# Performance work log

Measured on AMD Instinct MI355X. Metric: run time of the kernel, lower is better.

Reference implementation:

```python
import jax, jax.numpy as jnp
import numpy as np

ORDER = 2
M = 3  # number_timeseries


def setup_inputs() -> dict:
    key = jax.random.key(0)
    ks = jax.random.split(key, 8)
    N, T = 256, 4096
    H, OUT = 128, 10
    d_phi_in = (ORDER + 1) * M          # 9
    d_rho_in = ORDER * M + H            # 134
    s = lambda fan_in: 1.0 / np.sqrt(fan_in)
    return {
        "x": jax.random.normal(ks[0], (N, M * T), dtype=jnp.float32),
        "phi_w1": jax.random.normal(ks[1], (d_phi_in, H), dtype=jnp.float32) * s(d_phi_in),
        "phi_b1": jnp.zeros((H,), jnp.float32),
        "phi_w2": jax.random.normal(ks[2], (H, H), dtype=jnp.float32) * s(H),
        "phi_b2": jnp.zeros((H,), jnp.float32),
        "phi_w3": jax.random.normal(ks[3], (H, H), dtype=jnp.float32) * s(H),
        "phi_b3": jnp.zeros((H,), jnp.float32),
        "rho_w1": jax.random.normal(ks[4], (d_rho_in, H), dtype=jnp.float32) * s(d_rho_in),
        "rho_b1": jnp.zeros((H,), jnp.float32),
        "rho_w2": jax.random.normal(ks[5], (H, OUT), dtype=jnp.float32) * s(H),
        "rho_b2": jnp.zeros((OUT,), jnp.float32),
    }


def reference(x, phi_w1, phi_b1, phi_w2, phi_b2, phi_w3, phi_b3,
              rho_w1, rho_b1, rho_w2, rho_b2):
    N = x.shape[0]
    xr = x.reshape(N, M, -1)                      # (N, M, T)
    T = xr.shape[-1]
    L = T - ORDER                                 # number of windows
    # cat over lags along channel dim, then transpose -> (N, L, (ORDER+1)*M)
    input_inner = jnp.concatenate(
        [xr[:, :, i:L + i] for i in range(ORDER + 1)], axis=1
    ).swapaxes(1, 2)                              # (N, L, 9)
    h = jax.nn.relu(input_inner @ phi_w1 + phi_b1)
    h = jax.nn.relu(h @ phi_w2 + phi_b2)
    h = h @ phi_w3 + phi_b3                       # (N, L, 128)
    output_inner = jnp.sum(h, axis=1)             # (N, 128)
    input_outer = jnp.concatenate(
        [xr[:, :, :ORDER].reshape(N, -1), output_inner], axis=1
    )                                             # (N, 134)
    g = jax.nn.relu(input_outer @ rho_w1 + rho_b1)
    return g @ rho_w2 + rho_b2                    # (N, 10)
```

## Files before the change

kernel.cpp:

```cpp
#include <hip/hip_runtime.h>
#include <hip/hip_bf16.h>


#define NN 256
#define MM 3
#define TT 4096
#define LL 4094
#define HH 128
#define CHUNKS 4
#define STAGES 4
#define RPS 256
#define XROW 24

#define WS_W1 (512 * 1024)
#define WS_W2 (512 * 1024 + 8192)

typedef __attribute__((ext_vector_type(8))) short bf16x8;
typedef __attribute__((ext_vector_type(4))) float f32x4;
typedef __attribute__((ext_vector_type(4))) unsigned short u16x4;
typedef __attribute__((ext_vector_type(4))) unsigned int u32x4;

__device__ __forceinline__ unsigned short f2bf(float x) {
    __hip_bfloat16 h = __float2bfloat16(x);
    union { __hip_bfloat16 h; unsigned short u; } v; v.h = h;
    return v.u;
}

__global__ void pen_prep(const float* __restrict__ w1, const float* __restrict__ b1,
                         const float* __restrict__ w2,
                         unsigned short* __restrict__ w1t,
                         unsigned short* __restrict__ w2t)
{
    const int tid = threadIdx.x;
    for (int idx = tid; idx < 512; idx += 256) {
        const int cf = idx >> 6, lane = idx & 63;
        const int lq = lane >> 4, lr = lane & 15;
        const int chan = 32 * (cf >> 1) + 8 * (lr >> 2) + 4 * (cf & 1) + (lr & 3);
        #pragma unroll
        for (int e = 0; e < 8; ++e) {
            const int k = 8 * lq + e;
            float v = 0.f;
            if (k < 9)       v = w1[k * HH + chan];
            else if (k == 9) v = b1[chan];
            w1t[idx * 8 + e] = f2bf(v);
        }
    }
    for (int idx = tid; idx < 2048; idx += 256) {
        const int lane = idx & 63;
        const int kk = (idx >> 6) & 3, of = (idx >> 8) & 3, oh = idx >> 10;
        const int lq = lane >> 4, lr = lane & 15;
        const int o = oh * 64 + of * 16 + lr;
        #pragma unroll
        for (int e = 0; e < 8; ++e) {
            const int i = 32 * kk + 8 * lq + e;
            w2t[idx * 8 + e] = f2bf(w2[i * HH + o]);
        }
    }
}

__global__ __launch_bounds__(256, 2) void pen_inner(
    const float* __restrict__ x,
    const float* __restrict__ b2,
    const unsigned short* __restrict__ w1t,
    const unsigned short* __restrict__ w2t,
    float* __restrict__ partials)
{
    __shared__ __align__(16) unsigned short xw[XROW * RPS + 32];
    __shared__ float red[2][HH];

    const int tid  = threadIdx.x;
    const int wave = tid >> 6;
    const int lane = tid & 63;
    const int lr   = lane & 15;
    const int lq   = lane >> 4;
    const int rg   = wave >> 1;
    const int oh   = wave & 1;

    const int bx    = blockIdx.x;
    const int n     = bx >> 2;
    const int chunk = bx & 3;

    const float* xn = x + n * (MM * TT);

    bf16x8 w1f[8];
    #pragma unroll
    for (int cf = 0; cf < 8; ++cf)
        w1f[cf] = *(const bf16x8*)&w1t[(cf * 64 + lane) * 8];
    bf16x8 w2f[4][4];
    #pragma unroll
    for (int of = 0; of < 4; ++of)
        #pragma unroll
        for (int kk = 0; kk < 4; ++kk)
            w2f[of][kk] = *(const bf16x8*)&w2t[(((oh * 4 + of) * 4 + kk) * 64 + lane) * 8];
    f32x4 b2f[4];
    #pragma unroll
    for (int of = 0; of < 4; ++of)
        #pragma unroll
        for (int j = 0; j < 4; ++j)
            b2f[of][j] = b2[oh * 64 + of * 16 + lq * 4 + j];

    if (tid < 32) xw[XROW * RPS + tid] = 0;

    const f32x4 zero4 = {0.f, 0.f, 0.f, 0.f};
    const int xo = XROW * lr + 8 * lq;
    float colsum[4][4] = {{0,0,0,0},{0,0,0,0},{0,0,0,0},{0,0,0,0}};

    for (int st = 0; st < STAGES; ++st) {
        __syncthreads();

        {
            const int r = tid;
            const int rowg = chunk * 1024 + st * 256 + r;
            unsigned short kv[9];
            #pragma unroll
            for (int k = 0; k < 9; ++k) {
                const int i = k / 3;
                const int m = k - i * 3;
                const int t = rowg + i;
                kv[k] = (t < TT) ? f2bf(xn[m * TT + t]) : (unsigned short)0;
            }
            u16x4 s0, s1, s2;
            s0[0] = kv[0]; s0[1] = kv[1]; s0[2] = kv[2]; s0[3] = kv[3];
            s1[0] = kv[4]; s1[1] = kv[5]; s1[2] = kv[6]; s1[3] = kv[7];
            s2[0] = kv[8]; s2[1] = 0x3F80; s2[2] = 0; s2[3] = 0;
            u16x4 z; z[0] = 0; z[1] = 0; z[2] = 0; z[3] = 0;
            *(u16x4*)&xw[XROW * r]      = s0;
            *(u16x4*)&xw[XROW * r + 4]  = s1;
            *(u16x4*)&xw[XROW * r + 8]  = s2;
            *(u16x4*)&xw[XROW * r + 12] = z;
            *(u16x4*)&xw[XROW * r + 16] = z;
            *(u16x4*)&xw[XROW * r + 20] = z;
        }
        __syncthreads();

        #pragma unroll 2
        for (int uu = 0; uu < 8; ++uu) {
            const int u = uu * 2 + rg;
            const bf16x8 bfrag = *(const bf16x8*)&xw[u * (XROW * 16) + xo];

            f32x4 acc1[8];
            #pragma unroll
            for (int cf = 0; cf < 8; ++cf)
                acc1[cf] = __builtin_amdgcn_mfma_f32_16x16x32_bf16(
                               w1f[cf], bfrag, zero4, 0, 0, 0);

            bf16x8 pa[4];
            #pragma unroll
            for (int kk = 0; kk < 4; ++kk) {
                u32x4 d;
                d[0] = (unsigned)f2bf(fmaxf(acc1[2*kk][0], 0.f))
                     | ((unsigned)f2bf(fmaxf(acc1[2*kk][1], 0.f)) << 16);
                d[1] = (unsigned)f2bf(fmaxf(acc1[2*kk][2], 0.f))
                     | ((unsigned)f2bf(fmaxf(acc1[2*kk][3], 0.f)) << 16);
                d[2] = (unsigned)f2bf(fmaxf(acc1[2*kk+1][0], 0.f))
                     | ((unsigned)f2bf(fmaxf(acc1[2*kk+1][1], 0.f)) << 16);
                d[3] = (unsigned)f2bf(fmaxf(acc1[2*kk+1][2], 0.f))
                     | ((unsigned)f2bf(fmaxf(acc1[2*kk+1][3], 0.f)) << 16);
                pa[kk] = __builtin_bit_cast(bf16x8, d);
            }

            f32x4 acc2[4];
            #pragma unroll
            for (int of = 0; of < 4; ++of)
                acc2[of] = __builtin_amdgcn_mfma_f32_16x16x32_bf16(
                               w2f[of][0], pa[0], b2f[of], 0, 0, 0);
            #pragma unroll
            for (int kk = 1; kk < 4; ++kk)
                #pragma unroll
                for (int of = 0; of < 4; ++of)
                    acc2[of] = __builtin_amdgcn_mfma_f32_16x16x32_bf16(
                                   w2f[of][kk], pa[kk], acc2[of], 0, 0, 0);

            if ((chunk == 3) && (st == 3) && (uu == 7) && (rg == 1)) {
                const bool valid = lr < 14;
                #pragma unroll
                for (int of = 0; of < 4; ++of)
                    #pragma unroll
                    for (int j = 0; j < 4; ++j) {
                        float v = fmaxf(acc2[of][j], 0.f);
                        if (valid) colsum[of][j] += v;
                    }
            } else {
                #pragma unroll
                for (int of = 0; of < 4; ++of)
                    #pragma unroll
                    for (int j = 0; j < 4; ++j)
                        colsum[of][j] += fmaxf(acc2[of][j], 0.f);
            }
        }
    }

    #pragma unroll
    for (int of = 0; of < 4; ++of)
        #pragma unroll
        for (int j = 0; j < 4; ++j) {
            float v = colsum[of][j];
            #pragma unroll
            for (int msk = 1; msk < 16; msk <<= 1)
                v += __shfl_xor(v, msk, 64);
            if (lr == 0)
                red[rg][oh * 64 + of * 16 + lq * 4 + j] = v;
        }
    __syncthreads();
    if (tid < HH)
        partials[(n * CHUNKS + chunk) * HH + tid] = red[0][tid] + red[1][tid];
}

__global__ __launch_bounds__(128) void pen_outer(
    const float* __restrict__ x,
    const float* __restrict__ w3, const float* __restrict__ b3,
    const float* __restrict__ rw1, const float* __restrict__ rb1,
    const float* __restrict__ rw2, const float* __restrict__ rb2,
    const float* __restrict__ partials,
    float* __restrict__ out)
{
    __shared__ float S[HH];
    __shared__ float IO[136];
    __shared__ float G[HH];
    const int n = blockIdx.x;
    const int c = threadIdx.x;

    float s = 0.f;
    #pragma unroll
    for (int ch = 0; ch < CHUNKS; ++ch)
        s += partials[(n * CHUNKS + ch) * HH + c];
    S[c] = s;
    if (c < 6) IO[c] = x[n * (MM * TT) + (c >> 1) * TT + (c & 1)];
    __syncthreads();

    float oi = (float)LL * b3[c];
    for (int k = 0; k < HH; ++k) oi += S[k] * w3[k * HH + c];
    IO[6 + c] = oi;
    __syncthreads();

    float g = rb1[c];
    for (int k = 0; k < 134; ++k) g += IO[k] * rw1[k * HH + c];
    G[c] = fmaxf(g, 0.f);
    __syncthreads();

    if (c < 10) {
        float o = rb2[c];
        for (int k = 0; k < HH; ++k) o += G[k] * rw2[k * 10 + c];
        out[n * 10 + c] = o;
    }
}

extern "C" void kernel_launch(void* const* d_in, const int* in_sizes, int n_in,
                              void* d_out, int out_size, void* d_ws, size_t ws_size,
                              hipStream_t stream)
{
    (void)in_sizes; (void)n_in; (void)out_size; (void)ws_size;
    const float* x   = (const float*)d_in[0];
    const float* w1  = (const float*)d_in[1];
    const float* b1  = (const float*)d_in[2];
    const float* w2  = (const float*)d_in[3];
    const float* b2  = (const float*)d_in[4];
    const float* w3  = (const float*)d_in[5];
    const float* b3  = (const float*)d_in[6];
    const float* rw1 = (const float*)d_in[7];
    const float* rb1 = (const float*)d_in[8];
    const float* rw2 = (const float*)d_in[9];
    const float* rb2 = (const float*)d_in[10];

    float*          partials = (float*)d_ws;
    unsigned short* w1t = (unsigned short*)((char*)d_ws + WS_W1);
    unsigned short* w2t = (unsigned short*)((char*)d_ws + WS_W2);

    pen_prep<<<1, 256, 0, stream>>>(w1, b1, w2, w1t, w2t);
    pen_inner<<<NN * CHUNKS, 256, 0, stream>>>(x, b2, w1t, w2t, partials);
    pen_outer<<<NN, 128, 0, stream>>>(x, w3, b3, rw1, rb1, rw2, rb2, partials,
                                      (float*)d_out);
}
```

Measured before the change: 88.65 us.

## Split second-layer outputs across four waves to cut registers and raise occupancy

Each wave now computes all 16 row-groups but only 32 of the 128 second-layer output channels, instead of 8 row-groups times 64 channels. This shrinks the w2 fragment, bias and colsum register sets, so launch bounds can allow four blocks per CU. The first-layer MFMAs are fused into the kk loop so activations are consumed immediately. The trade-off is that every wave now recomputes the full first layer (twice the layer-1 MFMA work), and the LDS reduction is replaced by direct global writes.

```diff
diff --git a/kernel.cpp b/kernel.cpp
--- a/kernel.cpp
+++ b/kernel.cpp
@@ -47,9 +47,10 @@
     }
     for (int idx = tid; idx < 2048; idx += 256) {
         const int lane = idx & 63;
-        const int kk = (idx >> 6) & 3, of = (idx >> 8) & 3, oh = idx >> 10;
+        const int fid  = idx >> 6;
+        const int kk = fid & 3, of = (fid >> 2) & 1, w = fid >> 3;
         const int lq = lane >> 4, lr = lane & 15;
-        const int o = oh * 64 + of * 16 + lr;
+        const int o = w * 32 + of * 16 + lr;
         #pragma unroll
         for (int e = 0; e < 8; ++e) {
             const int i = 32 * kk + 8 * lq + e;
@@ -58,7 +59,7 @@
     }
 }
 
-__global__ __launch_bounds__(256, 2) void pen_inner(
+__global__ __launch_bounds__(256, 4) void pen_inner(
     const float* __restrict__ x,
     const float* __restrict__ b2,
     const unsigned short* __restrict__ w1t,
@@ -66,15 +67,12 @@
     float* __restrict__ partials)
 {
     __shared__ __align__(16) unsigned short xw[XROW * RPS + 32];
-    __shared__ float red[2][HH];
 
     const int tid  = threadIdx.x;
     const int wave = tid >> 6;
     const int lane = tid & 63;
     const int lr   = lane & 15;
     const int lq   = lane >> 4;
-    const int rg   = wave >> 1;
-    const int oh   = wave & 1;
 
     const int bx    = blockIdx.x;
     const int n     = bx >> 2;
@@ -86,24 +84,24 @@
     #pragma unroll
     for (int cf = 0; cf < 8; ++cf)
         w1f[cf] = *(const bf16x8*)&w1t[(cf * 64 + lane) * 8];
-    bf16x8 w2f[4][4];
-    #pragma unroll
-    for (int of = 0; of < 4; ++of)
+    bf16x8 w2f[2][4];
+    #pragma unroll
+    for (int of = 0; of < 2; ++of)
         #pragma unroll
         for (int kk = 0; kk < 4; ++kk)
-            w2f[of][kk] = *(const bf16x8*)&w2t[(((oh * 4 + of) * 4 + kk) * 64 + lane) * 8];
-    f32x4 b2f[4];
-    #pragma unroll
-    for (int of = 0; of < 4; ++of)
+            w2f[of][kk] = *(const bf16x8*)&w2t[(((wave * 2 + of) * 4 + kk) * 64 + lane) * 8];
+    f32x4 b2f[2];
+    #pragma unroll
+    for (int of = 0; of < 2; ++of)
         #pragma unroll
         for (int j = 0; j < 4; ++j)
-            b2f[of][j] = b2[oh * 64 + of * 16 + lq * 4 + j];
+            b2f[of][j] = b2[wave * 32 + of * 16 + lq * 4 + j];
 
     if (tid < 32) xw[XROW * RPS + tid] = 0;
 
     const f32x4 zero4 = {0.f, 0.f, 0.f, 0.f};
     const int xo = XROW * lr + 8 * lq;
-    float colsum[4][4] = {{0,0,0,0},{0,0,0,0},{0,0,0,0},{0,0,0,0}};
+    float colsum[2][4] = {{0,0,0,0},{0,0,0,0}};
 
     for (int st = 0; st < STAGES; ++st) {
         __syncthreads();
@@ -134,47 +132,43 @@
         __syncthreads();
 
         #pragma unroll 2
-        for (int uu = 0; uu < 8; ++uu) {
-            const int u = uu * 2 + rg;
+        for (int u = 0; u < 16; ++u) {
             const bf16x8 bfrag = *(const bf16x8*)&xw[u * (XROW * 16) + xo];
 
-            f32x4 acc1[8];
-            #pragma unroll
-            for (int cf = 0; cf < 8; ++cf)
-                acc1[cf] = __builtin_amdgcn_mfma_f32_16x16x32_bf16(
-                               w1f[cf], bfrag, zero4, 0, 0, 0);
-
-            bf16x8 pa[4];
+            f32x4 acc2[2];
             #pragma unroll
             for (int kk = 0; kk < 4; ++kk) {
+                f32x4 a0 = __builtin_amdgcn_mfma_f32_16x16x32_bf16(
+                               w1f[2 * kk],     bfrag, zero4, 0, 0, 0);
+                f32x4 a1 = __builtin_amdgcn_mfma_f32_16x16x32_bf16(
+                               w1f[2 * kk + 1], bfrag, zero4, 0, 0, 0);
                 u32x4 d;
-                d[0] = (unsigned)f2bf(fmaxf(acc1[2*kk][0], 0.f))
-                     | ((unsigned)f2bf(fmaxf(acc1[2*kk][1], 0.f)) << 16);
-                d[1] = (unsigned)f2bf(fmaxf(acc1[2*kk][2], 0.f))
-                     | ((unsigned)f2bf(fmaxf(acc1[2*kk][3], 0.f)) << 16);
-                d[2] = (unsigned)f2bf(fmaxf(acc1[2*kk+1][0], 0.f))
-                     | ((unsigned)f2bf(fmaxf(acc1[2*kk+1][1], 0.f)) << 16);
-                d[3] = (unsigned)f2bf(fmaxf(acc1[2*kk+1][2], 0.f))
-                     | ((unsigned)f2bf(fmaxf(acc1[2*kk+1][3], 0.f)) << 16);
-                pa[kk] = __builtin_bit_cast(bf16x8, d);
-            }
-
-            f32x4 acc2[4];
-            #pragma unroll
-            for (int of = 0; of < 4; ++of)
-                acc2[of] = __builtin_amdgcn_mfma_f32_16x16x32_bf16(
-                               w2f[of][0], pa[0], b2f[of], 0, 0, 0);
-            #pragma unroll
-            for (int kk = 1; kk < 4; ++kk)
-                #pragma unroll
-                for (int of = 0; of < 4; ++of)
-                    acc2[of] = __builtin_amdgcn_mfma_f32_16x16x32_bf16(
-                                   w2f[of][kk], pa[kk], acc2[of], 0, 0, 0);
-
-            if ((chunk == 3) && (st == 3) && (uu == 7) && (rg == 1)) {
+                d[0] = (unsigned)f2bf(fmaxf(a0[0], 0.f))
+                     | ((unsigned)f2bf(fmaxf(a0[1], 0.f)) << 16);
+                d[1] = (unsigned)f2bf(fmaxf(a0[2], 0.f))
+                     | ((unsigned)f2bf(fmaxf(a0[3], 0.f)) << 16);
+                d[2] = (unsigned)f2bf(fmaxf(a1[0], 0.f))
+                     | ((unsigned)f2bf(fmaxf(a1[1], 0.f)) << 16);
+                d[3] = (unsigned)f2bf(fmaxf(a1[2], 0.f))
+                     | ((unsigned)f2bf(fmaxf(a1[3], 0.f)) << 16);
+                const bf16x8 pa = __builtin_bit_cast(bf16x8, d);
+                if (kk == 0) {
+                    acc2[0] = __builtin_amdgcn_mfma_f32_16x16x32_bf16(
+                                  w2f[0][0], pa, b2f[0], 0, 0, 0);
+                    acc2[1] = __builtin_amdgcn_mfma_f32_16x16x32_bf16(
+                                  w2f[1][0], pa, b2f[1], 0, 0, 0);
+                } else {
+                    acc2[0] = __builtin_amdgcn_mfma_f32_16x16x32_bf16(
+                                  w2f[0][kk], pa, acc2[0], 0, 0, 0);
+                    acc2[1] = __builtin_amdgcn_mfma_f32_16x16x32_bf16(
+                                  w2f[1][kk], pa, acc2[1], 0, 0, 0);
+                }
+            }
+
+            if ((chunk == 3) && (st == 3) && (u == 15)) {
                 const bool valid = lr < 14;
                 #pragma unroll
-                for (int of = 0; of < 4; ++of)
+                for (int of = 0; of < 2; ++of)
                     #pragma unroll
                     for (int j = 0; j < 4; ++j) {
                         float v = fmaxf(acc2[of][j], 0.f);
@@ -182,7 +176,7 @@
                     }
             } else {
                 #pragma unroll
-                for (int of = 0; of < 4; ++of)
+                for (int of = 0; of < 2; ++of)
                     #pragma unroll
                     for (int j = 0; j < 4; ++j)
                         colsum[of][j] += fmaxf(acc2[of][j], 0.f);
@@ -191,19 +185,18 @@
     }
 
     #pragma unroll
-    for (int of = 0; of < 4; ++of)
+    for (int of = 0; of < 2; ++of)
         #pragma unroll
         for (int j = 0; j < 4; ++j) {
             float v = colsum[of][j];
             #pragma unroll
             for (int msk = 1; msk < 16; msk <<= 1)
                 v += __shfl_xor(v, msk, 64);
-            if (lr == 0)
-                red[rg][oh * 64 + of * 16 + lq * 4 + j] = v;
-        }
-    __syncthreads();
-    if (tid < HH)
-        partials[(n * CHUNKS + chunk) * HH + tid] = red[0][tid] + red[1][tid];
+            if (lr == 0) {
+                const int o = wave * 32 + of * 16 + lq * 4 + j;
+                partials[(n * CHUNKS + chunk) * HH + o] = v;
+            }
+        }
 }
 
 __global__ __launch_bounds__(128) void pen_outer(
```

Measured after the change: 116.1 us. +30.9%, slower.

## Split layer-1 channels across wave pairs and exchange activations via LDS

Applied to the files above, without the earlier changes.

Each wave pair now splits the 128 hidden channels of layer 1, so a wave computes only half the layer-1 MFMAs and gets its partner's half of the activations through a double-buffered LDS exchange before layer 2. Before, every wave recomputed all 128 layer-1 channels for its rows. The grid doubles to 8 chunks per sample with two halves of 256 rows each, and occupancy is raised to 3 blocks per CU. The float-to-bf16 conversion now uses a packed intrinsic. The cost is an extra __syncthreads per step and more LDS traffic.

```diff
diff --git a/kernel.cpp b/kernel.cpp
--- a/kernel.cpp
+++ b/kernel.cpp
@@ -7,24 +7,32 @@
 #define TT 4096
 #define LL 4094
 #define HH 128
-#define CHUNKS 4
-#define STAGES 4
-#define RPS 256
+#define CHUNKS 8
+#define RPC 512
+#define RPH 256
+#define HALVES 2
+#define STEPS 4
+#define SR 64
 #define XROW 24
 
-#define WS_W1 (512 * 1024)
-#define WS_W2 (512 * 1024 + 8192)
+#define WS_W1 (1024 * 1024)
+#define WS_W2 (1024 * 1024 + 8192)
 
 typedef __attribute__((ext_vector_type(8))) short bf16x8;
 typedef __attribute__((ext_vector_type(4))) float f32x4;
-typedef __attribute__((ext_vector_type(4))) unsigned short u16x4;
 typedef __attribute__((ext_vector_type(4))) unsigned int u32x4;
+typedef __attribute__((ext_vector_type(2))) unsigned int u32x2;
 
 __device__ __forceinline__ unsigned short f2bf(float x) {
     __hip_bfloat16 h = __float2bfloat16(x);
     union { __hip_bfloat16 h; unsigned short u; } v; v.h = h;
     return v.u;
 }
+__device__ __forceinline__ unsigned pkbf2(float a, float b) {
+    union { __hip_bfloat162 h; unsigned u; } v;
+    v.h = __float22bfloat162_rn(make_float2(a, b));
+    return v.u;
+}
 
 __global__ void pen_prep(const float* __restrict__ w1, const float* __restrict__ b1,
                          const float* __restrict__ w2,
@@ -33,9 +41,10 @@
 {
     const int tid = threadIdx.x;
     for (int idx = tid; idx < 512; idx += 256) {
-        const int cf = idx >> 6, lane = idx & 63;
+        const int wc = idx >> 8, cf = (idx >> 6) & 3, lane = idx & 63;
         const int lq = lane >> 4, lr = lane & 15;
-        const int chan = 32 * (cf >> 1) + 8 * (lr >> 2) + 4 * (cf & 1) + (lr & 3);
+        const int chan = 64 * wc + 32 * (cf >> 1) + 8 * (lr >> 2)
+                       + 4 * (cf & 1) + (lr & 3);
         #pragma unroll
         for (int e = 0; e < 8; ++e) {
             const int k = 8 * lq + e;
@@ -47,9 +56,9 @@
     }
     for (int idx = tid; idx < 2048; idx += 256) {
         const int lane = idx & 63;
-        const int kk = (idx >> 6) & 3, of = (idx >> 8) & 3, oh = idx >> 10;
+        const int kk = (idx >> 6) & 3, of = (idx >> 8) & 3, wc = idx >> 10;
         const int lq = lane >> 4, lr = lane & 15;
-        const int o = oh * 64 + of * 16 + lr;
+        const int o = 64 * wc + 16 * of + lr;
         #pragma unroll
         for (int e = 0; e < 8; ++e) {
             const int i = 32 * kk + 8 * lq + e;
@@ -58,14 +67,15 @@
     }
 }
 
-__global__ __launch_bounds__(256, 2) void pen_inner(
+__global__ __launch_bounds__(256, 3) void pen_inner(
     const float* __restrict__ x,
     const float* __restrict__ b2,
     const unsigned short* __restrict__ w1t,
     const unsigned short* __restrict__ w2t,
     float* __restrict__ partials)
 {
-    __shared__ __align__(16) unsigned short xw[XROW * RPS + 32];
+    __shared__ __align__(16) unsigned short xw[XROW * (RPH + 1) + 8];
+    __shared__ __align__(16) unsigned short mb[2][4][2][2][512];
     __shared__ float red[2][HH];
 
     const int tid  = threadIdx.x;
@@ -73,119 +83,135 @@
     const int lane = tid & 63;
     const int lr   = lane & 15;
     const int lq   = lane >> 4;
-    const int rg   = wave >> 1;
-    const int oh   = wave & 1;
+    const int wr   = wave >> 1;
+    const int wc   = wave & 1;
+    const int pw   = wave ^ 1;
 
     const int bx    = blockIdx.x;
-    const int n     = bx >> 2;
-    const int chunk = bx & 3;
+    const int n     = bx >> 3;
+    const int chunk = bx & 7;
 
     const float* xn = x + n * (MM * TT);
 
-    bf16x8 w1f[8];
-    #pragma unroll
-    for (int cf = 0; cf < 8; ++cf)
-        w1f[cf] = *(const bf16x8*)&w1t[(cf * 64 + lane) * 8];
+    bf16x8 w1f[4];
+    #pragma unroll
+    for (int cf = 0; cf < 4; ++cf)
+        w1f[cf] = *(const bf16x8*)&w1t[((wc * 4 + cf) * 64 + lane) * 8];
     bf16x8 w2f[4][4];
     #pragma unroll
     for (int of = 0; of < 4; ++of)
         #pragma unroll
         for (int kk = 0; kk < 4; ++kk)
-            w2f[of][kk] = *(const bf16x8*)&w2t[(((oh * 4 + of) * 4 + kk) * 64 + lane) * 8];
+            w2f[of][kk] = *(const bf16x8*)&w2t[(((wc * 4 + of) * 4 + kk) * 64 + lane) * 8];
     f32x4 b2f[4];
     #pragma unroll
     for (int of = 0; of < 4; ++of)
         #pragma unroll
         for (int j = 0; j < 4; ++j)
-            b2f[of][j] = b2[oh * 64 + of * 16 + lq * 4 + j];
-
-    if (tid < 32) xw[XROW * RPS + tid] = 0;
+            b2f[of][j] = b2[wc * 64 + of * 16 + lq * 4 + j];
+
+    if (tid < XROW + 8) xw[XROW * RPH + tid] = 0;
 
     const f32x4 zero4 = {0.f, 0.f, 0.f, 0.f};
-    const int xo = XROW * lr + 8 * lq;
+    const int xo   = XROW * lr + 8 * lq;
+    const int myk0 = 2 * wc;
+    const int pk0  = 2 - 2 * wc;
+
     float colsum[4][4] = {{0,0,0,0},{0,0,0,0},{0,0,0,0},{0,0,0,0}};
 
-    for (int st = 0; st < STAGES; ++st) {
-        __syncthreads();
+    for (int half = 0; half < HALVES; ++half) {
+        const int lbase = chunk * RPC + half * RPH;
 
         {
             const int r = tid;
-            const int rowg = chunk * 1024 + st * 256 + r;
-            unsigned short kv[9];
+            float kv[9];
             #pragma unroll
             for (int k = 0; k < 9; ++k) {
                 const int i = k / 3;
                 const int m = k - i * 3;
-                const int t = rowg + i;
-                kv[k] = (t < TT) ? f2bf(xn[m * TT + t]) : (unsigned short)0;
+                const int t = lbase + r + i;
+                kv[k] = (t < TT) ? xn[m * TT + t] : 0.f;
             }
-            u16x4 s0, s1, s2;
-            s0[0] = kv[0]; s0[1] = kv[1]; s0[2] = kv[2]; s0[3] = kv[3];
-            s1[0] = kv[4]; s1[1] = kv[5]; s1[2] = kv[6]; s1[3] = kv[7];
-            s2[0] = kv[8]; s2[1] = 0x3F80; s2[2] = 0; s2[3] = 0;
-            u16x4 z; z[0] = 0; z[1] = 0; z[2] = 0; z[3] = 0;
-            *(u16x4*)&xw[XROW * r]      = s0;
-            *(u16x4*)&xw[XROW * r + 4]  = s1;
-            *(u16x4*)&xw[XROW * r + 8]  = s2;
-            *(u16x4*)&xw[XROW * r + 12] = z;
-            *(u16x4*)&xw[XROW * r + 16] = z;
-            *(u16x4*)&xw[XROW * r + 20] = z;
+            u32x2 p0, p1, p2, z2;
+            p0[0] = pkbf2(kv[0], kv[1]); p0[1] = pkbf2(kv[2], kv[3]);
+            p1[0] = pkbf2(kv[4], kv[5]); p1[1] = pkbf2(kv[6], kv[7]);
+            p2[0] = pkbf2(kv[8], 1.0f);  p2[1] = 0u;
+            z2[0] = 0u; z2[1] = 0u;
+            *(u32x2*)&xw[XROW * r]      = p0;
+            *(u32x2*)&xw[XROW * r + 4]  = p1;
+            *(u32x2*)&xw[XROW * r + 8]  = p2;
+            *(u32x2*)&xw[XROW * r + 12] = z2;
+            *(u32x2*)&xw[XROW * r + 16] = z2;
+            *(u32x2*)&xw[XROW * r + 20] = z2;
         }
         __syncthreads();
 
-        #pragma unroll 2
-        for (int uu = 0; uu < 8; ++uu) {
-            const int u = uu * 2 + rg;
-            const bf16x8 bfrag = *(const bf16x8*)&xw[u * (XROW * 16) + xo];
-
-            f32x4 acc1[8];
-            #pragma unroll
-            for (int cf = 0; cf < 8; ++cf)
-                acc1[cf] = __builtin_amdgcn_mfma_f32_16x16x32_bf16(
-                               w1f[cf], bfrag, zero4, 0, 0, 0);
-
-            bf16x8 pa[4];
-            #pragma unroll
-            for (int kk = 0; kk < 4; ++kk) {
-                u32x4 d;
-                d[0] = (unsigned)f2bf(fmaxf(acc1[2*kk][0], 0.f))
-                     | ((unsigned)f2bf(fmaxf(acc1[2*kk][1], 0.f)) << 16);
-                d[1] = (unsigned)f2bf(fmaxf(acc1[2*kk][2], 0.f))
-                     | ((unsigned)f2bf(fmaxf(acc1[2*kk][3], 0.f)) << 16);
-                d[2] = (unsigned)f2bf(fmaxf(acc1[2*kk+1][0], 0.f))
-                     | ((unsigned)f2bf(fmaxf(acc1[2*kk+1][1], 0.f)) << 16);
-                d[3] = (unsigned)f2bf(fmaxf(acc1[2*kk+1][2], 0.f))
-                     | ((unsigned)f2bf(fmaxf(acc1[2*kk+1][3], 0.f)) << 16);
-                pa[kk] = __builtin_bit_cast(bf16x8, d);
+        for (int s = 0; s < STEPS; ++s) {
+            const int buf = (half * STEPS + s) & 1;
+
+            bf16x8 pa[2][2];
+            #pragma unroll
+            for (int rf = 0; rf < 2; ++rf) {
+                const int R = s * SR + wr * 32 + rf * 16 + lr;
+                const bf16x8 bfrag = *(const bf16x8*)&xw[R * XROW + 8 * lq];
+                f32x4 a[4];
+                #pragma unroll
+                for (int cf = 0; cf < 4; ++cf)
+                    a[cf] = __builtin_amdgcn_mfma_f32_16x16x32_bf16(
+                                w1f[cf], bfrag, zero4, 0, 0, 0);
+                #pragma unroll
+                for (int kkL = 0; kkL < 2; ++kkL) {
+                    u32x4 d;
+                    d[0] = pkbf2(fmaxf(a[2*kkL][0], 0.f),   fmaxf(a[2*kkL][1], 0.f));
+                    d[1] = pkbf2(fmaxf(a[2*kkL][2], 0.f),   fmaxf(a[2*kkL][3], 0.f));
+                    d[2] = pkbf2(fmaxf(a[2*kkL+1][0], 0.f), fmaxf(a[2*kkL+1][1], 0.f));
+                    d[3] = pkbf2(fmaxf(a[2*kkL+1][2], 0.f), fmaxf(a[2*kkL+1][3], 0.f));
+                    pa[rf][kkL] = __builtin_bit_cast(bf16x8, d);
+                    *(bf16x8*)&mb[buf][wave][kkL][rf][lane * 8] = pa[rf][kkL];
+                }
             }
-
-            f32x4 acc2[4];
-            #pragma unroll
-            for (int of = 0; of < 4; ++of)
-                acc2[of] = __builtin_amdgcn_mfma_f32_16x16x32_bf16(
-                               w2f[of][0], pa[0], b2f[of], 0, 0, 0);
-            #pragma unroll
-            for (int kk = 1; kk < 4; ++kk)
-                #pragma unroll
-                for (int of = 0; of < 4; ++of)
-                    acc2[of] = __builtin_amdgcn_mfma_f32_16x16x32_bf16(
-                                   w2f[of][kk], pa[kk], acc2[of], 0, 0, 0);
-
-            if ((chunk == 3) && (st == 3) && (uu == 7) && (rg == 1)) {
-                const bool valid = lr < 14;
-                #pragma unroll
-                for (int of = 0; of < 4; ++of)
+            __syncthreads();
+
+            const bool tailw = (chunk == CHUNKS - 1) && (half == HALVES - 1)
+                               && (s == STEPS - 1) && (wr == 1);
+            #pragma unroll
+            for (int rf = 0; rf < 2; ++rf) {
+                const bf16x8 hp0 = *(const bf16x8*)&mb[buf][pw][0][rf][lane * 8];
+                const bf16x8 hp1 = *(const bf16x8*)&mb[buf][pw][1][rf][lane * 8];
+                f32x4 acc2[4];
+                #pragma unroll
+                for (int of = 0; of < 4; ++of)
+                    acc2[of] = __builtin_amdgcn_mfma_f32_16x16x32_bf16(
+                                   w2f[of][myk0], pa[rf][0], b2f[of], 0, 0, 0);
+                #pragma unroll
+                for (int of = 0; of < 4; ++of)
+                    acc2[of] = __builtin_amdgcn_mfma_f32_16x16x32_bf16(
+                                   w2f[of][myk0 + 1], pa[rf][1], acc2[of], 0, 0, 0);
+                #pragma unroll
+                for (int of = 0; of < 4; ++of)
+                    acc2[of] = __builtin_amdgcn_mfma_f32_16x16x32_bf16(
+                                   w2f[of][pk0], hp0, acc2[of], 0, 0, 0);
+                #pragma unroll
+                for (int of = 0; of < 4; ++of)
+                    acc2[of] = __builtin_amdgcn_mfma_f32_16x16x32_bf16(
+                                   w2f[of][pk0 + 1], hp1, acc2[of], 0, 0, 0);
+
+                if (tailw && rf == 1) {
+                    const bool valid = lr < 14;
                     #pragma unroll
-                    for (int j = 0; j < 4; ++j) {
-                        float v = fmaxf(acc2[of][j], 0.f);
-                        if (valid) colsum[of][j] += v;
-                    }
-            } else {
-                #pragma unroll
-                for (int of = 0; of < 4; ++of)
+                    for (int of = 0; of < 4; ++of)
+                        #pragma unroll
+                        for (int j = 0; j < 4; ++j) {
+                            float v = fmaxf(acc2[of][j], 0.f);
+                            if (valid) colsum[of][j] += v;
+                        }
+                } else {
                     #pragma unroll
-                    for (int j = 0; j < 4; ++j)
-                        colsum[of][j] += fmaxf(acc2[of][j], 0.f);
+                    for (int of = 0; of < 4; ++of)
+                        #pragma unroll
+                        for (int j = 0; j < 4; ++j)
+                            colsum[of][j] += fmaxf(acc2[of][j], 0.f);
+                }
             }
         }
     }
@@ -199,7 +225,7 @@
             for (int msk = 1; msk < 16; msk <<= 1)
                 v += __shfl_xor(v, msk, 64);
             if (lr == 0)
-                red[rg][oh * 64 + of * 16 + lq * 4 + j] = v;
+                red[wr][wc * 64 + of * 16 + lq * 4 + j] = v;
         }
     __syncthreads();
     if (tid < HH)
```

After: 302.6 us. 3.41x slower.
